# Performance work log

Hardware: AMD Instinct MI355X
Metric: run time of the kernel (lower is better)

The kernel has to match this reference:

```python
import jax, jax.numpy as jnp
import numpy as np

NUM_LAYERS = 24      # controller steps (architecture layers)
NUM_ACTIONS = 16
LSTM_SIZE = 2048
LSTM_NUM_LAYERS = 2


def setup_inputs() -> dict:
    key = jax.random.key(0)
    ks = jax.random.split(key, 7)
    H, A, L = LSTM_SIZE, NUM_ACTIONS, LSTM_NUM_LAYERS
    s = 0.05  # init scale to keep gates unsaturated
    return {
        "g_emb": jax.random.normal(ks[0], (1, H), jnp.float32) * s,
        "w_emb": jax.random.normal(ks[1], (A, H), jnp.float32) * s,
        "soft_w": jax.random.normal(ks[2], (H, A), jnp.float32) * s,
        "w_ih": jax.random.normal(ks[3], (L, 4 * H, H), jnp.float32) * s,
        "w_hh": jax.random.normal(ks[4], (L, 4 * H, H), jnp.float32) * s,
        "b_ih": jax.random.normal(ks[5], (L, 4 * H), jnp.float32) * s,
        "b_hh": jax.random.normal(ks[6], (L, 4 * H), jnp.float32) * s,
    }


def _controller(g_emb, w_emb, soft_w, w_ih, w_hh, b_ih, b_hh):
    H, L = LSTM_SIZE, LSTM_NUM_LAYERS
    sample_keys = jax.random.split(jax.random.key(42), NUM_LAYERS)

    def lstm_stack(x, h, c):
        # x: [1,H]; h, c: [L,1,H]. PyTorch gate order: i, f, g, o.
        h_new, c_new = [], []
        for l in range(L):
            gates = x @ w_ih[l].T + h[l] @ w_hh[l].T + b_ih[l] + b_hh[l]  # [1,4H]
            i_g, f_g, g_g, o_g = jnp.split(gates, 4, axis=-1)
            c_l = jax.nn.sigmoid(f_g) * c[l] + jax.nn.sigmoid(i_g) * jnp.tanh(g_g)
            h_l = jax.nn.sigmoid(o_g) * jnp.tanh(c_l)
            h_new.append(h_l)
            c_new.append(c_l)
            x = h_l
        return x, jnp.stack(h_new), jnp.stack(c_new)

    def step(carry, k):
        x, h, c = carry
        out, h, c = lstm_stack(x, h, c)          # out: [1,H]
        logits = (out @ soft_w)[0]               # [A]
        action = jax.random.categorical(k, logits)
        logp = jax.nn.log_softmax(logits)
        lp = logp[action]
        ent = -jnp.sum(jnp.exp(logp) * logp)
        x_next = w_emb[action][None, :]          # [1,H]
        return (x_next, h, c), (action, lp, ent)

    h0 = jnp.zeros((L, 1, H), g_emb.dtype)
    c0 = jnp.zeros((L, 1, H), g_emb.dtype)
    _, (actions, logprobs, entropies) = jax.lax.scan(step, (g_emb, h0, c0), sample_keys)
    return actions, logprobs, entropies


def reference(g_emb, w_emb, soft_w, w_ih, w_hh, b_ih, b_hh):
    # Returns (sampled architecture actions [num_layers] int,
    #          per-step log-probs [num_layers], per-step entropies [num_layers]).
    return _controller(g_emb, w_emb, soft_w, w_ih, w_hh, b_ih, b_hh)
```

## Files before the change

### kernel.cpp

```cpp
#include <hip/hip_runtime.h>
#include <math.h>

#define HD 2048
#define NACT 16
#define NSTEP 24
#define WL (4*HD*HD)
#define NIH (2*WL)

#define NWG 256
#define NTHR 512
#define NWG_FB 256
#define NTHR_FB 512

typedef float  nf4 __attribute__((ext_vector_type(4)));

__device__ __forceinline__ float ld_agent(const float* p) {
  return __hip_atomic_load(p, __ATOMIC_RELAXED, __HIP_MEMORY_SCOPE_AGENT);
}
__device__ __forceinline__ float2 ld_agent2(const float* p) {
  unsigned long long v = __hip_atomic_load((const unsigned long long*)p,
                                           __ATOMIC_RELAXED, __HIP_MEMORY_SCOPE_AGENT);
  float2 r;
  r.x = __uint_as_float((unsigned)v);
  r.y = __uint_as_float((unsigned)(v >> 32));
  return r;
}
__device__ __forceinline__ void st_agent(float* p, float v) {
  __hip_atomic_store(p, v, __ATOMIC_RELAXED, __HIP_MEMORY_SCOPE_AGENT);
}

__device__ __forceinline__ unsigned rotl32(unsigned v, int r) { return (v << r) | (v >> (32 - r)); }

__device__ __forceinline__ void threefry(unsigned k0, unsigned k1, unsigned x0, unsigned x1,
                                         unsigned& o0, unsigned& o1) {
  unsigned ks2 = k0 ^ k1 ^ 0x1BD11BDAu;
#define TFR(r) { x0 += x1; x1 = rotl32(x1, r); x1 ^= x0; }
  x0 += k0; x1 += k1;
  TFR(13) TFR(15) TFR(26) TFR(6)
  x0 += k1;  x1 += ks2 + 1u;
  TFR(17) TFR(29) TFR(16) TFR(24)
  x0 += ks2; x1 += k0 + 2u;
  TFR(13) TFR(15) TFR(26) TFR(6)
  x0 += k0;  x1 += k1 + 3u;
  TFR(17) TFR(29) TFR(16) TFR(24)
  x0 += k1;  x1 += ks2 + 4u;
  TFR(13) TFR(15) TFR(26) TFR(6)
  x0 += ks2; x1 += k0 + 5u;
#undef TFR
  o0 = x0; o1 = x1;
}

__device__ __forceinline__ float sigmoidf(float x) { return 1.0f / (1.0f + expf(-x)); }

__device__ __forceinline__ unsigned f2bf(float f) {
  unsigned u = __float_as_uint(f);
  return (u + 0x7fffu + ((u >> 16) & 1u)) >> 16;
}
#define BF_LO(u) __uint_as_float((u) << 16)
#define BF_HI(u) __uint_as_float((u) & 0xffff0000u)

__device__ void grid_bar(unsigned* flags, unsigned* release, unsigned ep) {
  __syncthreads();
  if (threadIdx.x == 0) {
    __hip_atomic_store(&flags[blockIdx.x], ep, __ATOMIC_RELAXED, __HIP_MEMORY_SCOPE_AGENT);
  }
  if (blockIdx.x == 0) {
    if (threadIdx.x < 64) {
      const unsigned* my = flags + threadIdx.x * 4;
      long guard = 0;
      for (;;) {
        unsigned f0 = __hip_atomic_load(my + 0, __ATOMIC_RELAXED, __HIP_MEMORY_SCOPE_AGENT);
        unsigned f1 = __hip_atomic_load(my + 1, __ATOMIC_RELAXED, __HIP_MEMORY_SCOPE_AGENT);
        unsigned f2 = __hip_atomic_load(my + 2, __ATOMIC_RELAXED, __HIP_MEMORY_SCOPE_AGENT);
        unsigned f3 = __hip_atomic_load(my + 3, __ATOMIC_RELAXED, __HIP_MEMORY_SCOPE_AGENT);
        bool ok = (f0 >= ep) && (f1 >= ep) && (f2 >= ep) && (f3 >= ep);
        if (__all(ok)) break;
        if (++guard > 1000000L) break;
        __builtin_amdgcn_s_sleep(2);
      }
      if (threadIdx.x == 0) {
        __hip_atomic_store(release, ep, __ATOMIC_RELAXED, __HIP_MEMORY_SCOPE_AGENT);
      }
    }
  } else {
    if (threadIdx.x == 0) {
      long guard = 0;
      while (__hip_atomic_load(release, __ATOMIC_RELAXED, __HIP_MEMORY_SCOPE_AGENT) < ep &&
             guard < 1000000L) {
        __builtin_amdgcn_s_sleep(4);
        ++guard;
      }
    }
  }
  __syncthreads();
}

__device__ int sample_step(const float* __restrict__ h1g, const float* __restrict__ soft_w,
                           int t, float* lp_out, float* ent_out) {
  __shared__ float s_part[8][NACT];
  __shared__ float s_res[3];
  const int wave = threadIdx.x >> 6;
  const int lane = threadIdx.x & 63;

  float lg[NACT];
#pragma unroll
  for (int a = 0; a < NACT; ++a) lg[a] = 0.0f;
#pragma unroll
  for (int m = 0; m < 2; ++m) {
    int p = wave * 128 + m * 64 + lane;
    float2 hv = ld_agent2(h1g + p * 2);
    const float* sw0 = soft_w + (size_t)(p * 2) * NACT;
    const float* sw1 = sw0 + NACT;
#pragma unroll
    for (int h = 0; h < 2; ++h) {
      const float* sw = h ? sw1 : sw0;
      float hvv = h ? hv.y : hv.x;
      float4 r0 = *(const float4*)(sw);
      float4 r1 = *(const float4*)(sw + 4);
      float4 r2 = *(const float4*)(sw + 8);
      float4 r3 = *(const float4*)(sw + 12);
      lg[0]  += hvv * r0.x; lg[1]  += hvv * r0.y; lg[2]  += hvv * r0.z; lg[3]  += hvv * r0.w;
      lg[4]  += hvv * r1.x; lg[5]  += hvv * r1.y; lg[6]  += hvv * r1.z; lg[7]  += hvv * r1.w;
      lg[8]  += hvv * r2.x; lg[9]  += hvv * r2.y; lg[10] += hvv * r2.z; lg[11] += hvv * r2.w;
      lg[12] += hvv * r3.x; lg[13] += hvv * r3.y; lg[14] += hvv * r3.z; lg[15] += hvv * r3.w;
    }
  }
#pragma unroll
  for (int off = 32; off > 0; off >>= 1) {
#pragma unroll
    for (int a = 0; a < NACT; ++a) lg[a] += __shfl_xor(lg[a], off, 64);
  }
  if (lane == 0) {
#pragma unroll
    for (int a = 0; a < NACT; ++a) s_part[wave][a] = lg[a];
  }
  __syncthreads();

  if (wave == 0 && lane < NACT) {
    float logit = 0.0f;
#pragma unroll
    for (int w = 0; w < 8; ++w) logit += s_part[w][lane];

    unsigned kt0, kt1, b0, b1;
    threefry(0u, 42u, 0u, (unsigned)t, kt0, kt1);
    threefry(kt0, kt1, 0u, (unsigned)lane, b0, b1);
    unsigned bits = b0 ^ b1;

    const float tiny = 1.17549435e-38f;
    float u = __uint_as_float((bits >> 9) | 0x3f800000u) - 1.0f;
    u = fmaxf(tiny, u + tiny);
    float gmb = -logf(-logf(u));
    float z = logit + gmb;

    int idx = lane; float zz = z;
#pragma unroll
    for (int off = 8; off > 0; off >>= 1) {
      float oz = __shfl_xor(zz, off, NACT);
      int   oi = __shfl_xor(idx, off, NACT);
      if (oz > zz || (oz == zz && oi < idx)) { zz = oz; idx = oi; }
    }
    float mx = logit;
#pragma unroll
    for (int off = 8; off > 0; off >>= 1) mx = fmaxf(mx, __shfl_xor(mx, off, NACT));
    float sh = logit - mx;
    float se = expf(sh);
#pragma unroll
    for (int off = 8; off > 0; off >>= 1) se += __shfl_xor(se, off, NACT);
    float lp = sh - logf(se);
    float term = expf(lp) * lp;
#pragma unroll
    for (int off = 8; off > 0; off >>= 1) term += __shfl_xor(term, off, NACT);
    float lp_sel = __shfl(lp, idx, NACT);
    if (lane == 0) { s_res[0] = (float)idx; s_res[1] = lp_sel; s_res[2] = -term; }
  }
  __syncthreads();
  int act = (int)s_res[0];
  *lp_out = s_res[1];
  *ent_out = s_res[2];
  return act;
}


__global__ void __launch_bounds__(256) conv_bf16(const float* __restrict__ src,
                                                 unsigned* __restrict__ dst) {
  size_t i = ((size_t)blockIdx.x * blockDim.x + threadIdx.x) * 8;
  const nf4* s4 = (const nf4*)(src + i);
  nf4 a = __builtin_nontemporal_load(s4);
  nf4 b = __builtin_nontemporal_load(s4 + 1);
  uint4 o;
  o.x = (f2bf(a.y) << 16) | f2bf(a.x);
  o.y = (f2bf(a.w) << 16) | f2bf(a.z);
  o.z = (f2bf(b.y) << 16) | f2bf(b.x);
  o.w = (f2bf(b.w) << 16) | f2bf(b.z);
  *(uint4*)(dst + i / 2) = o;
}

__device__ void layer_bf16(const unsigned* __restrict__ wiL, const unsigned* __restrict__ whL,
                           const float* __restrict__ bihL, const float* __restrict__ bhhL,
                           const float* __restrict__ x, bool x_is_shared_state,
                           const float* __restrict__ hin,
                           float* __restrict__ hout, float* __restrict__ c,
                           float* s_x, float* s_h) {
  const int tid = threadIdx.x;
  if (x_is_shared_state) {
    float2 a = ld_agent2(x + tid * 2);
    float2 b = ld_agent2(x + 1024 + tid * 2);
    *(float2*)(s_x + tid * 2) = a;
    *(float2*)(s_x + 1024 + tid * 2) = b;
  } else {
    *(float4*)(s_x + tid * 4) = *(const float4*)(x + tid * 4);
  }
  {
    float2 ha = ld_agent2(hin + tid * 2);
    float2 hb = ld_agent2(hin + 1024 + tid * 2);
    *(float2*)(s_h + tid * 2) = ha;
    *(float2*)(s_h + 1024 + tid * 2) = hb;
  }
  __syncthreads();

  const int wave = tid >> 6;
  const int lane = tid & 63;
  const int j = (int)blockIdx.x * 8 + wave;

  float4 xv[8], hv[8];
#pragma unroll
  for (int k = 0; k < 8; ++k) {
    int e = k * 256 + lane * 4;
    xv[k] = *(const float4*)(s_x + e);
    hv[k] = *(const float4*)(s_h + e);
  }

  float acc[4];
#pragma unroll
  for (int g = 0; g < 4; ++g) {
    const unsigned* wi = wiL + ((size_t)(g * HD + j) * HD >> 1);
    const unsigned* wh = whL + ((size_t)(g * HD + j) * HD >> 1);
    float si = 0.0f, sh2 = 0.0f;
#pragma unroll
    for (int k = 0; k < 8; ++k) {
      int e2 = k * 128 + lane * 2;
      uint2 qa = *(const uint2*)(wi + e2);
      uint2 qb = *(const uint2*)(wh + e2);
      si  += BF_LO(qa.x) * xv[k].x + BF_HI(qa.x) * xv[k].y;
      si  += BF_LO(qa.y) * xv[k].z + BF_HI(qa.y) * xv[k].w;
      sh2 += BF_LO(qb.x) * hv[k].x + BF_HI(qb.x) * hv[k].y;
      sh2 += BF_LO(qb.y) * hv[k].z + BF_HI(qb.y) * hv[k].w;
    }
    acc[g] = si + sh2;
  }
#pragma unroll
  for (int off = 32; off > 0; off >>= 1) {
#pragma unroll
    for (int g = 0; g < 4; ++g) acc[g] += __shfl_xor(acc[g], off, 64);
  }
  if (lane == 0) {
    float gi = acc[0] + bihL[j]          + bhhL[j];
    float gf = acc[1] + bihL[HD + j]     + bhhL[HD + j];
    float gg = acc[2] + bihL[2 * HD + j] + bhhL[2 * HD + j];
    float go = acc[3] + bihL[3 * HD + j] + bhhL[3 * HD + j];
    float cn = sigmoidf(gf) * c[j] + sigmoidf(gi) * tanhf(gg);
    c[j] = cn;
    st_agent(&hout[j], sigmoidf(go) * tanhf(cn));
  }
}

__global__ void __launch_bounds__(NTHR) ctrl2_kernel(
    const float* __restrict__ g_emb, const float* __restrict__ w_emb,
    const float* __restrict__ soft_w,
    const unsigned* __restrict__ wb_ih, const unsigned* __restrict__ wb_hh,
    const float* __restrict__ b_ih, const float* __restrict__ b_hh,
    float* __restrict__ out, float* __restrict__ state,
    unsigned* __restrict__ flags, unsigned* __restrict__ release) {
  __shared__ float s_x[HD];
  __shared__ float s_h[HD];
  float* h0 = state;
  float* h1 = state + 2 * HD;
  float* c0 = state + 4 * HD;
  float* c1 = state + 5 * HD;

  if (threadIdx.x < 8) {
    int j = (int)blockIdx.x * 8 + (int)threadIdx.x;
    st_agent(&h0[j], 0.0f); st_agent(&h1[j], 0.0f);
    c0[j] = 0.0f; c1[j] = 0.0f;
  }
  unsigned ep = 1;
  grid_bar(flags, release, ep++);

  const unsigned* wi0 = wb_ih;             const unsigned* wh0 = wb_hh;
  const unsigned* wi1 = wb_ih + WL / 2;    const unsigned* wh1 = wb_hh + WL / 2;

  const float* x = g_emb;
  for (int t = 0; t < NSTEP; ++t) {
    int q = t & 1;
    layer_bf16(wi0, wh0, b_ih, b_hh, x, false,
               h0 + q * HD, h0 + (1 - q) * HD, c0, s_x, s_h);
    grid_bar(flags, release, ep++);
    layer_bf16(wi1, wh1, b_ih + 4 * HD, b_hh + 4 * HD,
               h0 + (1 - q) * HD, true,
               h1 + q * HD, h1 + (1 - q) * HD, c1, s_x, s_h);
    grid_bar(flags, release, ep++);
    float lp, en;
    int act = sample_step(h1 + (1 - q) * HD, soft_w, t, &lp, &en);
    if (blockIdx.x == 0 && threadIdx.x == 0) {
      out[t] = (float)act;
      out[NSTEP + t] = lp;
      out[2 * NSTEP + t] = en;
    }
    x = w_emb + (size_t)act * HD;
  }
}


__device__ void grid_bar_ctr(unsigned long long* ctr, unsigned long long target) {
  __syncthreads();
  if (threadIdx.x == 0) {
    __builtin_amdgcn_fence(__ATOMIC_SEQ_CST, "agent");
    __hip_atomic_fetch_add(ctr, 1ull, __ATOMIC_RELAXED, __HIP_MEMORY_SCOPE_AGENT);
    long guard = 0;
    while (__hip_atomic_load(ctr, __ATOMIC_RELAXED, __HIP_MEMORY_SCOPE_AGENT) < target &&
           guard < 20000000L) {
      __builtin_amdgcn_s_sleep(2);
      ++guard;
    }
    __builtin_amdgcn_fence(__ATOMIC_SEQ_CST, "agent");
  }
  __syncthreads();
}

__device__ int sample_step8(const float* __restrict__ h1g, const float* __restrict__ soft_w,
                            int t, float* lp_out, float* ent_out) {
  __shared__ float s_part[8][NACT];
  __shared__ float s_res[3];
  const int wave = threadIdx.x >> 6;
  const int lane = threadIdx.x & 63;

  float lg[NACT];
#pragma unroll
  for (int a = 0; a < NACT; ++a) lg[a] = 0.0f;
#pragma unroll
  for (int m = 0; m < 4; ++m) {
    int e = wave * 256 + m * 64 + lane;
    float hv = h1g[e];
    const float* sw = soft_w + (size_t)e * NACT;
    float4 r0 = *(const float4*)(sw);
    float4 r1 = *(const float4*)(sw + 4);
    float4 r2 = *(const float4*)(sw + 8);
    float4 r3 = *(const float4*)(sw + 12);
    lg[0]  += hv * r0.x; lg[1]  += hv * r0.y; lg[2]  += hv * r0.z; lg[3]  += hv * r0.w;
    lg[4]  += hv * r1.x; lg[5]  += hv * r1.y; lg[6]  += hv * r1.z; lg[7]  += hv * r1.w;
    lg[8]  += hv * r2.x; lg[9]  += hv * r2.y; lg[10] += hv * r2.z; lg[11] += hv * r2.w;
    lg[12] += hv * r3.x; lg[13] += hv * r3.y; lg[14] += hv * r3.z; lg[15] += hv * r3.w;
  }
#pragma unroll
  for (int off = 32; off > 0; off >>= 1) {
#pragma unroll
    for (int a = 0; a < NACT; ++a) lg[a] += __shfl_xor(lg[a], off, 64);
  }
  if (lane == 0) {
#pragma unroll
    for (int a = 0; a < NACT; ++a) s_part[wave][a] = lg[a];
  }
  __syncthreads();

  if (wave == 0 && lane < NACT) {
    float logit = 0.0f;
#pragma unroll
    for (int w = 0; w < 8; ++w) logit += s_part[w][lane];
    unsigned kt0, kt1, b0, b1;
    threefry(0u, 42u, 0u, (unsigned)t, kt0, kt1);
    threefry(kt0, kt1, 0u, (unsigned)lane, b0, b1);
    unsigned bits = b0 ^ b1;
    const float tiny = 1.17549435e-38f;
    float u = __uint_as_float((bits >> 9) | 0x3f800000u) - 1.0f;
    u = fmaxf(tiny, u + tiny);
    float gmb = -logf(-logf(u));
    float z = logit + gmb;
    int idx = lane; float zz = z;
#pragma unroll
    for (int off = 8; off > 0; off >>= 1) {
      float oz = __shfl_xor(zz, off, NACT);
      int   oi = __shfl_xor(idx, off, NACT);
      if (oz > zz || (oz == zz && oi < idx)) { zz = oz; idx = oi; }
    }
    float mx = logit;
#pragma unroll
    for (int off = 8; off > 0; off >>= 1) mx = fmaxf(mx, __shfl_xor(mx, off, NACT));
    float sh = logit - mx;
    float se = expf(sh);
#pragma unroll
    for (int off = 8; off > 0; off >>= 1) se += __shfl_xor(se, off, NACT);
    float lp = sh - logf(se);
    float term = expf(lp) * lp;
#pragma unroll
    for (int off = 8; off > 0; off >>= 1) term += __shfl_xor(term, off, NACT);
    float lp_sel = __shfl(lp, idx, NACT);
    if (lane == 0) { s_res[0] = (float)idx; s_res[1] = lp_sel; s_res[2] = -term; }
  }
  __syncthreads();
  int act = (int)s_res[0];
  *lp_out = s_res[1];
  *ent_out = s_res[2];
  return act;
}

__device__ void lstm_layer(const float* __restrict__ Wih, const float* __restrict__ Whh,
                           const float* __restrict__ bih, const float* __restrict__ bhh,
                           const float* __restrict__ x, const float* __restrict__ hin,
                           float* __restrict__ hout, float* __restrict__ c) {
  const int wave = threadIdx.x >> 6;
  const int lane = threadIdx.x & 63;
  const int j = (int)blockIdx.x * 8 + wave;

  float4 xv[8], hv[8];
#pragma unroll
  for (int k = 0; k < 8; ++k) {
    int e = k * 256 + lane * 4;
    xv[k] = *(const float4*)(x + e);
    hv[k] = *(const float4*)(hin + e);
  }
  float acc[4];
#pragma unroll
  for (int g = 0; g < 4; ++g) {
    const float* wi = Wih + (size_t)(g * HD + j) * HD;
    const float* wh = Whh + (size_t)(g * HD + j) * HD;
    float s = 0.0f;
#pragma unroll
    for (int k = 0; k < 8; ++k) {
      int e = k * 256 + lane * 4;
      float4 a4 = *(const float4*)(wi + e);
      float4 b4 = *(const float4*)(wh + e);
      s += a4.x * xv[k].x; s += a4.y * xv[k].y; s += a4.z * xv[k].z; s += a4.w * xv[k].w;
      s += b4.x * hv[k].x; s += b4.y * hv[k].y; s += b4.z * hv[k].z; s += b4.w * hv[k].w;
    }
    acc[g] = s;
  }
#pragma unroll
  for (int off = 32; off > 0; off >>= 1) {
#pragma unroll
    for (int g = 0; g < 4; ++g) acc[g] += __shfl_xor(acc[g], off, 64);
  }
  if (lane == 0) {
    float gi = acc[0] + bih[j]          + bhh[j];
    float gf = acc[1] + bih[HD + j]     + bhh[HD + j];
    float gg = acc[2] + bih[2 * HD + j] + bhh[2 * HD + j];
    float go = acc[3] + bih[3 * HD + j] + bhh[3 * HD + j];
    float cn = sigmoidf(gf) * c[j] + sigmoidf(gi) * tanhf(gg);
    c[j] = cn;
    hout[j] = sigmoidf(go) * tanhf(cn);
  }
}

__global__ void __launch_bounds__(NTHR_FB) ctrl_kernel(
    const float* __restrict__ g_emb, const float* __restrict__ w_emb,
    const float* __restrict__ soft_w, const float* __restrict__ w_ih,
    const float* __restrict__ w_hh, const float* __restrict__ b_ih,
    const float* __restrict__ b_hh, float* __restrict__ out, float* __restrict__ ws) {
  float* h0 = ws;
  float* h1 = ws + 2 * HD;
  float* c0 = ws + 4 * HD;
  float* c1 = ws + 5 * HD;
  unsigned long long* bar = (unsigned long long*)(ws + 6 * HD);

  if (threadIdx.x < 8) {
    int j = (int)blockIdx.x * 8 + (int)threadIdx.x;
    h0[j] = 0.0f; h1[j] = 0.0f; c0[j] = 0.0f; c1[j] = 0.0f;
  }
  unsigned long long ep = 1;
  grid_bar_ctr(bar, (ep++) * NWG_FB);

  const float* x = g_emb;
  for (int t = 0; t < NSTEP; ++t) {
    int q = t & 1;
    lstm_layer(w_ih, w_hh, b_ih, b_hh, x, h0 + q * HD, h0 + (1 - q) * HD, c0);
    grid_bar_ctr(bar, (ep++) * NWG_FB);
    lstm_layer(w_ih + WL, w_hh + WL, b_ih + 4 * HD, b_hh + 4 * HD,
               h0 + (1 - q) * HD, h1 + q * HD, h1 + (1 - q) * HD, c1);
    grid_bar_ctr(bar, (ep++) * NWG_FB);
    float lp, en;
    int act = sample_step8(h1 + (1 - q) * HD, soft_w, t, &lp, &en);
    if (blockIdx.x == 0 && threadIdx.x == 0) {
      out[t] = (float)act;
      out[NSTEP + t] = lp;
      out[2 * NSTEP + t] = en;
    }
    x = w_emb + (size_t)act * HD;
  }
}

__global__ void init_sync(unsigned* flags) {
  flags[threadIdx.x] = 0u;
}
__global__ void init_bar(unsigned long long* bar) { *bar = 0ull; }

extern "C" void kernel_launch(void* const* d_in, const int* in_sizes, int n_in,
                              void* d_out, int out_size, void* d_ws, size_t ws_size,
                              hipStream_t stream) {
  const float* g_emb  = (const float*)d_in[0];
  const float* w_emb  = (const float*)d_in[1];
  const float* soft_w = (const float*)d_in[2];
  const float* w_ih   = (const float*)d_in[3];
  const float* w_hh   = (const float*)d_in[4];
  const float* b_ih   = (const float*)d_in[5];
  const float* b_hh   = (const float*)d_in[6];

  const size_t wbytes = (size_t)NIH * 2 * sizeof(unsigned short);
  const size_t need = wbytes + (size_t)6 * HD * sizeof(float) + 512 * sizeof(unsigned) + 64;

  if (ws_size >= need) {
    unsigned* wb_ih = (unsigned*)d_ws;
    unsigned* wb_hh = wb_ih + NIH / 2;
    float* state = (float*)((char*)d_ws + wbytes);
    unsigned* flags = (unsigned*)(state + 6 * HD);
    unsigned* release = flags + 320;

    hipLaunchKernelGGL(init_sync, dim3(1), dim3(512), 0, stream, flags);
    hipLaunchKernelGGL(conv_bf16, dim3(NIH / (256 * 8)), dim3(256), 0, stream, w_ih, wb_ih);
    hipLaunchKernelGGL(conv_bf16, dim3(NIH / (256 * 8)), dim3(256), 0, stream, w_hh, wb_hh);
    hipLaunchKernelGGL(ctrl2_kernel, dim3(NWG), dim3(NTHR), 0, stream,
                       g_emb, w_emb, soft_w, wb_ih, wb_hh, b_ih, b_hh,
                       (float*)d_out, state, flags, release);
  } else {
    float* ws = (float*)d_ws;
    unsigned long long* bar = (unsigned long long*)(ws + 6 * HD);
    hipLaunchKernelGGL(init_bar, dim3(1), dim3(1), 0, stream, bar);
    hipLaunchKernelGGL(ctrl_kernel, dim3(NWG_FB), dim3(NTHR_FB), 0, stream,
                       g_emb, w_emb, soft_w, w_ih, w_hh, b_ih, b_hh,
                       (float*)d_out, ws);
  }
}
```

Baseline: 851.2 us.

## Prefetch next phase's bf16 weight rows into LDS across grid barriers

Each wave now streams its gate weight rows into a per-wave LDS buffer with global_load_lds, double-buffering two gates at a time. It issues the first two gates of the next layer's rows before the grid barrier, so weight fetch latency overlaps barrier waiting and the sampling step. This adds 128KB of LDS per block, which limits occupancy to one block per CU. It also depends on manual vmcnt waits and sched barriers being correct.

```diff
diff --git a/kernel.cpp b/kernel.cpp
--- a/kernel.cpp
+++ b/kernel.cpp
@@ -13,6 +13,8 @@
 #define NTHR_FB 512
 
 typedef float  nf4 __attribute__((ext_vector_type(4)));
+typedef const void __attribute__((address_space(1))) gas_void;
+typedef void __attribute__((address_space(3))) las_void;
 
 __device__ __forceinline__ float ld_agent(const float* p) {
   return __hip_atomic_load(p, __ATOMIC_RELAXED, __HIP_MEMORY_SCOPE_AGENT);
@@ -28,6 +30,14 @@
 __device__ __forceinline__ void st_agent(float* p, float v) {
   __hip_atomic_store(p, v, __ATOMIC_RELAXED, __HIP_MEMORY_SCOPE_AGENT);
 }
+
+__device__ __forceinline__ void gl16(const unsigned* g, unsigned* l) {
+  __builtin_amdgcn_global_load_lds((gas_void*)g, (las_void*)l, 16, 0, 0);
+}
+
+#define WAITVM8 { asm volatile("s_waitcnt vmcnt(8)" ::: "memory"); __builtin_amdgcn_sched_barrier(0); }
+#define WAITVM0 { asm volatile("s_waitcnt vmcnt(0)" ::: "memory"); __builtin_amdgcn_sched_barrier(0); }
+#define SB      { __builtin_amdgcn_sched_barrier(0); }
 
 __device__ __forceinline__ unsigned rotl32(unsigned v, int r) { return (v << r) | (v >> (32 - r)); }
 
@@ -195,12 +205,40 @@
   *(uint4*)(dst + i / 2) = o;
 }
 
-__device__ void layer_bf16(const unsigned* __restrict__ wiL, const unsigned* __restrict__ whL,
-                           const float* __restrict__ bihL, const float* __restrict__ bhhL,
-                           const float* __restrict__ x, bool x_is_shared_state,
-                           const float* __restrict__ hin,
-                           float* __restrict__ hout, float* __restrict__ c,
-                           float* s_x, float* s_h) {
+__device__ __forceinline__ void row_prefetch(const unsigned* __restrict__ wrow,
+                                             unsigned* ldst, int lane) {
+#pragma unroll
+  for (int cc = 0; cc < 4; ++cc)
+    gl16(wrow + cc * 256 + lane * 4, ldst + cc * 256);
+}
+
+__device__ __forceinline__ float gate_dot(const unsigned* wbuf,
+                                          const float4* xv, const float4* hv, int lane) {
+  const unsigned* wi_l = wbuf;
+  const unsigned* wh_l = wbuf + 1024;
+  float si = 0.0f, sh2 = 0.0f;
+#pragma unroll
+  for (int k = 0; k < 8; ++k) {
+    uint2 qa = *(const uint2*)(wi_l + k * 128 + lane * 2);
+    uint2 qb = *(const uint2*)(wh_l + k * 128 + lane * 2);
+    si  += BF_LO(qa.x) * xv[k].x + BF_HI(qa.x) * xv[k].y;
+    si  += BF_LO(qa.y) * xv[k].z + BF_HI(qa.y) * xv[k].w;
+    sh2 += BF_LO(qb.x) * hv[k].x + BF_HI(qb.x) * hv[k].y;
+    sh2 += BF_LO(qb.y) * hv[k].z + BF_HI(qb.y) * hv[k].w;
+  }
+  return si + sh2;
+}
+
+#define GS (((size_t)HD * HD) >> 1)
+
+__device__ void layer_phase(const unsigned* __restrict__ wiL, const unsigned* __restrict__ whL,
+                            const unsigned* __restrict__ nwiL, const unsigned* __restrict__ nwhL,
+                            const float* __restrict__ bihL, const float* __restrict__ bhhL,
+                            const float* __restrict__ x, bool x_is_shared_state,
+                            const float* __restrict__ hin,
+                            float* __restrict__ hout, float* __restrict__ c,
+                            float* s_x, float* s_h, unsigned* s_wv,
+                            int j, int lane) {
   const int tid = threadIdx.x;
   if (x_is_shared_state) {
     float2 a = ld_agent2(x + tid * 2);
@@ -218,10 +256,6 @@
   }
   __syncthreads();
 
-  const int wave = tid >> 6;
-  const int lane = tid & 63;
-  const int j = (int)blockIdx.x * 8 + wave;
-
   float4 xv[8], hv[8];
 #pragma unroll
   for (int k = 0; k < 8; ++k) {
@@ -230,24 +264,27 @@
     hv[k] = *(const float4*)(s_h + e);
   }
 
+  const size_t jrow = (size_t)j * 1024;
   float acc[4];
-#pragma unroll
-  for (int g = 0; g < 4; ++g) {
-    const unsigned* wi = wiL + ((size_t)(g * HD + j) * HD >> 1);
-    const unsigned* wh = whL + ((size_t)(g * HD + j) * HD >> 1);
-    float si = 0.0f, sh2 = 0.0f;
-#pragma unroll
-    for (int k = 0; k < 8; ++k) {
-      int e2 = k * 128 + lane * 2;
-      uint2 qa = *(const uint2*)(wi + e2);
-      uint2 qb = *(const uint2*)(wh + e2);
-      si  += BF_LO(qa.x) * xv[k].x + BF_HI(qa.x) * xv[k].y;
-      si  += BF_LO(qa.y) * xv[k].z + BF_HI(qa.y) * xv[k].w;
-      sh2 += BF_LO(qb.x) * hv[k].x + BF_HI(qb.x) * hv[k].y;
-      sh2 += BF_LO(qb.y) * hv[k].z + BF_HI(qb.y) * hv[k].w;
-    }
-    acc[g] = si + sh2;
-  }
+
+  acc[0] = gate_dot(s_wv, xv, hv, lane);
+  SB;
+  row_prefetch(wiL + 2 * GS + jrow, s_wv, lane);
+  row_prefetch(whL + 2 * GS + jrow, s_wv + 1024, lane);
+  acc[1] = gate_dot(s_wv + 2048, xv, hv, lane);
+  SB;
+  row_prefetch(wiL + 3 * GS + jrow, s_wv + 2048, lane);
+  row_prefetch(whL + 3 * GS + jrow, s_wv + 3072, lane);
+  WAITVM8;
+  acc[2] = gate_dot(s_wv, xv, hv, lane);
+  WAITVM0;
+  acc[3] = gate_dot(s_wv + 2048, xv, hv, lane);
+  SB;
+  row_prefetch(nwiL + jrow, s_wv, lane);
+  row_prefetch(nwhL + jrow, s_wv + 1024, lane);
+  row_prefetch(nwiL + GS + jrow, s_wv + 2048, lane);
+  row_prefetch(nwhL + GS + jrow, s_wv + 3072, lane);
+
 #pragma unroll
   for (int off = 32; off > 0; off >>= 1) {
 #pragma unroll
@@ -273,35 +310,49 @@
     unsigned* __restrict__ flags, unsigned* __restrict__ release) {
   __shared__ float s_x[HD];
   __shared__ float s_h[HD];
+  __shared__ unsigned s_w[8 * 4096];
   float* h0 = state;
   float* h1 = state + 2 * HD;
   float* c0 = state + 4 * HD;
   float* c1 = state + 5 * HD;
 
-  if (threadIdx.x < 8) {
-    int j = (int)blockIdx.x * 8 + (int)threadIdx.x;
-    st_agent(&h0[j], 0.0f); st_agent(&h1[j], 0.0f);
-    c0[j] = 0.0f; c1[j] = 0.0f;
-  }
+  const int tid  = threadIdx.x;
+  const int wave = tid >> 6;
+  const int lane = tid & 63;
+  const int j = (int)blockIdx.x * 8 + wave;
+  unsigned* s_wv = s_w + wave * 4096;
+
+  if (tid < 8) {
+    int jj = (int)blockIdx.x * 8 + tid;
+    st_agent(&h0[jj], 0.0f); st_agent(&h1[jj], 0.0f);
+    c0[jj] = 0.0f; c1[jj] = 0.0f;
+  }
+
+  const unsigned* wi0 = wb_ih;             const unsigned* wh0 = wb_hh;
+  const unsigned* wi1 = wb_ih + WL / 2;    const unsigned* wh1 = wb_hh + WL / 2;
+  const size_t jrow = (size_t)j * 1024;
+
+  row_prefetch(wi0 + jrow, s_wv, lane);
+  row_prefetch(wh0 + jrow, s_wv + 1024, lane);
+  row_prefetch(wi0 + GS + jrow, s_wv + 2048, lane);
+  row_prefetch(wh0 + GS + jrow, s_wv + 3072, lane);
+
   unsigned ep = 1;
   grid_bar(flags, release, ep++);
-
-  const unsigned* wi0 = wb_ih;             const unsigned* wh0 = wb_hh;
-  const unsigned* wi1 = wb_ih + WL / 2;    const unsigned* wh1 = wb_hh + WL / 2;
 
   const float* x = g_emb;
   for (int t = 0; t < NSTEP; ++t) {
     int q = t & 1;
-    layer_bf16(wi0, wh0, b_ih, b_hh, x, false,
-               h0 + q * HD, h0 + (1 - q) * HD, c0, s_x, s_h);
+    layer_phase(wi0, wh0, wi1, wh1, b_ih, b_hh, x, false,
+                h0 + q * HD, h0 + (1 - q) * HD, c0, s_x, s_h, s_wv, j, lane);
     grid_bar(flags, release, ep++);
-    layer_bf16(wi1, wh1, b_ih + 4 * HD, b_hh + 4 * HD,
-               h0 + (1 - q) * HD, true,
-               h1 + q * HD, h1 + (1 - q) * HD, c1, s_x, s_h);
+    layer_phase(wi1, wh1, wi0, wh0, b_ih + 4 * HD, b_hh + 4 * HD,
+                h0 + (1 - q) * HD, true,
+                h1 + q * HD, h1 + (1 - q) * HD, c1, s_x, s_h, s_wv, j, lane);
     grid_bar(flags, release, ep++);
     float lp, en;
     int act = sample_step(h1 + (1 - q) * HD, soft_w, t, &lp, &en);
-    if (blockIdx.x == 0 && threadIdx.x == 0) {
+    if (blockIdx.x == 0 && tid == 0) {
       out[t] = (float)act;
       out[NSTEP + t] = lp;
       out[2 * NSTEP + t] = en;
```

Result: slower. 881.0 us (+3.5%).
